# Kernel optimization log

Hardware: AMD Instinct MI355X
Metric: run time of the kernel (lower is better)

The kernel has to match this reference:

```python
import jax, jax.numpy as jnp
from jax import lax
import numpy as np

FW = 30          # edge_filter_width
THRESH = 0.015   # point_thresh
TOPK = 2000
SCALE = 4        # scale_cood2feat


def setup_inputs() -> dict:
    key = jax.random.key(0)
    k1, k2, k3 = jax.random.split(key, 3)
    B, H, W, C = 32, 384, 640, 128
    prob_nms = jax.random.uniform(k1, (B, 1, H, W), dtype=jnp.float32)
    featmap = jax.random.normal(k2, (B, C, H // SCALE, W // SCALE), dtype=jnp.float32)
    ratio = jax.random.uniform(k3, (B, 1), dtype=jnp.float32, minval=0.5, maxval=1.5)
    r_shape = jnp.tile(jnp.array([[H, W]], dtype=jnp.int64), (B, 1))
    return {"prob_nms": prob_nms, "featmap": featmap, "ratio": ratio, "r_shape": r_shape}


def _bilinear_gather(feat_hwc, pts_xy):
    # feat_hwc: [Hf, Wf, C]; pts_xy: [K, 2] float pixel coords (x, y)
    cf = pts_xy / SCALE
    x, y = cf[:, 0], cf[:, 1]
    x0 = jnp.floor(x).astype(jnp.int32)
    y0 = jnp.floor(y).astype(jnp.int32)
    x1, y1 = x0 + 1, y0 + 1
    fx1, fy1 = x1.astype(cf.dtype), y1.astype(cf.dtype)
    fx0, fy0 = x0.astype(cf.dtype), y0.astype(cf.dtype)
    wa = ((fx1 - x) * (fy1 - y))[:, None]
    wb = ((fx1 - x) * (y - fy0))[:, None]
    wc = ((x - fx0) * (fy1 - y))[:, None]
    wd = ((x - fx0) * (y - fy0))[:, None]
    Ia = feat_hwc[y0, x0]
    Ib = feat_hwc[y1, x0]
    Ic = feat_hwc[y0, x1]
    Id = feat_hwc[y1, x1]
    return Ia * wa + Ib * wb + Ic * wc + Id * wd


def _post_process_one(prob_hw, feat_hwc, ratio_s, rshape):
    H, W = prob_hw.shape
    iy = jnp.arange(H)[:, None]
    ix = jnp.arange(W)[None, :]
    # edge filtering: borders set to -1 == excluded from threshold test
    in_region = (iy >= FW) & (iy < rshape[0] - FW) & (ix >= FW) & (ix < rshape[1] - FW)
    mask = in_region & (prob_hw > THRESH)
    # compaction in row-major order (same order torch.where yields), padded with H*W
    lin = jnp.arange(H * W, dtype=jnp.int32)
    sentinel = jnp.int32(H * W)
    vals = jnp.where(mask.reshape(-1), lin, sentinel)
    neg_top, _ = lax.top_k(-vals, TOPK)   # smallest TOPK values, ascending
    idx = -neg_top
    valid = idx < sentinel
    idx_c = jnp.where(valid, idx, 0)
    yc = idx_c // W
    xc = idx_c % W
    pts_xy = jnp.stack([xc, yc], axis=1).astype(feat_hwc.dtype)  # flip -> (x, y)
    des = _bilinear_gather(feat_hwc, pts_xy)
    pts = pts_xy / ratio_s
    pts = jnp.where(valid[:, None], pts, jnp.zeros((), pts.dtype))
    des = jnp.where(valid[:, None], des, jnp.zeros((), des.dtype))
    return pts, des


def reference(prob_nms, featmap, ratio, r_shape):
    prob = prob_nms[:, 0]                       # [B, H, W]
    feat = jnp.transpose(featmap, (0, 2, 3, 1)) # [B, Hf, Wf, C]
    pts_t, des_t = jax.vmap(_post_process_one)(prob, feat, ratio[:, 0], r_shape)
    return pts_t, des_t
```

## Files before the change

### kernel.cpp

```cpp
#include <hip/hip_runtime.h>

#define NB 32
#define H 384
#define W 640
#define NC 128
#define FH 96
#define FWID 160
#define BORDER 30
#define PTHRESH 0.015f
#define TOPK 2000
#define HW (H * W)
#define NWAVE 4
#define NXIT 10

__device__ inline void load_rshape(const int* p32, int b, int* rs0, int* rs1) {
  const int a = p32[2 * b];
  const int c = p32[2 * b + 1];
  if (c == 0) {
    const long long* p64 = (const long long*)p32;
    *rs0 = (int)p64[2 * b];
    *rs1 = (int)p64[2 * b + 1];
  } else {
    *rs0 = a;
    *rs1 = c;
  }
}

__global__ __launch_bounds__(256) void compact_kernel(
    const float* __restrict__ prob, const int* __restrict__ rsp,
    int* __restrict__ out, int stride) {
  const int b = blockIdx.x;
  const int tid = threadIdx.x;
  const int lane = tid & 63;
  const int wv = tid >> 6;
  int rs0, rs1;
  load_rshape(rsp, b, &rs0, &rs1);
  const int ymax = rs0 - BORDER;
  const int xmax = rs1 - BORDER;
  const float* pb = prob + (size_t)b * HW;
  int* ob = out + (size_t)b * TOPK * stride;
  const unsigned long long ltmask = (1ull << lane) - 1ull;

  __shared__ int s_cnt[NWAVE];

  int chunk_base = 0;
  for (int row0 = BORDER; row0 < ymax && chunk_base < TOPK; row0 += NWAVE) {
    const int r = row0 + wv;
    unsigned long long mbs[NXIT];
    int cnt = 0;
    if (r < ymax) {
      const float* rowp = pb + r * W;
#pragma unroll
      for (int t = 0; t < NXIT; ++t) {
        const int x = t * 64 + lane;
        const bool m = (x >= BORDER) && (x < xmax) && (rowp[x] > PTHRESH);
        mbs[t] = __ballot(m);
        cnt += __popcll(mbs[t]);
      }
    } else {
#pragma unroll
      for (int t = 0; t < NXIT; ++t) mbs[t] = 0;
    }
    if (lane == 0) s_cnt[wv] = cnt;
    __syncthreads();
    int row_start = chunk_base;
    int total = 0;
#pragma unroll
    for (int j = 0; j < NWAVE; ++j) {
      const int cj = s_cnt[j];
      if (j < wv) row_start += cj;
      total += cj;
    }
    if (cnt > 0 && row_start < TOPK) {
      int rank = row_start;
      const int ibase = r * W;
#pragma unroll
      for (int t = 0; t < NXIT; ++t) {
        const unsigned long long mb = mbs[t];
        const bool m = (mb >> lane) & 1ull;
        const int pos = rank + __popcll(mb & ltmask);
        if (m && pos < TOPK) ob[(size_t)pos * stride] = ibase + t * 64 + lane;
        rank += __popcll(mb);
      }
    }
    chunk_base += total;
    __syncthreads();
  }
  const int filled = chunk_base < TOPK ? chunk_base : TOPK;
  for (int k = filled + tid; k < TOPK; k += 256)
    ob[(size_t)k * stride] = HW;
}

__global__ __launch_bounds__(128) void gather_kernel(
    const float* __restrict__ featmap, const float* __restrict__ ratio,
    const int* __restrict__ idx_base, int stride, float* __restrict__ pts,
    float* __restrict__ des) {
  const int k = blockIdx.x;
  const int b = blockIdx.y;
  const int pk = b * TOPK + k;
  const int c = threadIdx.x;

  const int idx = idx_base[(size_t)pk * stride];
  __syncthreads();

  const bool valid = (unsigned)idx < (unsigned)HW;
  const int ic = valid ? idx : 0;
  const int y = ic / W;
  const int x = ic - y * W;
  const int x0 = x >> 2;
  const int y0 = y >> 2;
  const float fx = (float)(x & 3) * 0.25f;
  const float fy = (float)(y & 3) * 0.25f;
  const float gx = 1.0f - fx, gy = 1.0f - fy;
  const float wa = gx * gy, wb = gx * fy, wc = fx * gy, wd = fx * fy;

  const float* fp = featmap + (((size_t)b * NC + c) * FH + y0) * FWID + x0;
  const float Ia = fp[0];
  const float Ic = fp[1];
  const float Ib = fp[FWID];
  const float Id = fp[FWID + 1];
  const float v = Ia * wa + Ib * wb + Ic * wc + Id * wd;
  des[(size_t)pk * NC + c] = valid ? v : 0.0f;

  if (c < 2) {
    const float p = (c == 0 ? (float)x : (float)y) / ratio[b];
    pts[pk * 2 + c] = valid ? p : 0.0f;
  }
}

extern "C" void kernel_launch(void* const* d_in, const int* in_sizes, int n_in,
                              void* d_out, int out_size, void* d_ws,
                              size_t ws_size, hipStream_t stream) {
  const float* prob = (const float*)d_in[0];
  const float* featmap = (const float*)d_in[1];
  const float* ratio = (const float*)d_in[2];
  const int* r_shape = (const int*)d_in[3];

  float* pts = (float*)d_out;
  float* des = pts + (size_t)NB * TOPK * 2;

  int* idx_base;
  int stride;
  if (ws_size >= (size_t)NB * TOPK * sizeof(int)) {
    idx_base = (int*)d_ws;
    stride = 1;
  } else {
    idx_base = (int*)des;
    stride = NC;
  }

  compact_kernel<<<NB, 256, 0, stream>>>(prob, r_shape, idx_base, stride);
  dim3 ggrid(TOPK, NB);
  gather_kernel<<<ggrid, 128, 0, stream>>>(featmap, ratio, idx_base, stride,
                                           pts, des);
}
```

Baseline: 370.2 us.

## Tile gather over 64 points per block with shared-memory transpose for coalescing

The gather kernel moves from one block per point, with one thread per channel, to one block per 64-point tile. Lanes now map to points and waves loop over channels, so neighbouring lanes read adjacent featmap addresses within a channel plane. Results are staged in a padded shared-memory tile and then written out channel-contiguous, so the descriptor stores stay coalesced. This cuts the block count and the scattered per-channel loads, at the cost of about 33 KB of shared memory per block and an extra barrier.

Measured after the change: 326.0 us. 1.14x faster.

```diff
diff --git a/kernel.cpp b/kernel.cpp
--- a/kernel.cpp
+++ b/kernel.cpp
@@ -12,6 +12,8 @@
 #define HW (H * W)
 #define NWAVE 4
 #define NXIT 10
+#define PTILE 64
+#define NTILE ((TOPK + PTILE - 1) / PTILE)
 
 __device__ inline void load_rshape(const int* p32, int b, int* rs0, int* rs1) {
   const int a = p32[2 * b];
@@ -91,18 +93,27 @@
     ob[(size_t)k * stride] = HW;
 }
 
-__global__ __launch_bounds__(128) void gather_kernel(
+__global__ __launch_bounds__(256) void gather_kernel(
     const float* __restrict__ featmap, const float* __restrict__ ratio,
     const int* __restrict__ idx_base, int stride, float* __restrict__ pts,
     float* __restrict__ des) {
-  const int k = blockIdx.x;
+  const int tile = blockIdx.x;
   const int b = blockIdx.y;
-  const int pk = b * TOPK + k;
-  const int c = threadIdx.x;
+  const int k0 = tile * PTILE;
+  const int npts = (TOPK - k0) < PTILE ? (TOPK - k0) : PTILE;
+  const int pk0 = b * TOPK + k0;
+  const int tid = threadIdx.x;
+  const int lane = tid & 63;
+  const int wv = tid >> 6;
 
-  const int idx = idx_base[(size_t)pk * stride];
+  __shared__ int s_idx[PTILE];
+  __shared__ float s_tile[NC][PTILE + 1];
+
+  if (tid < PTILE)
+    s_idx[tid] = (tid < npts) ? idx_base[(size_t)(pk0 + tid) * stride] : HW;
   __syncthreads();
 
+  const int idx = s_idx[lane];
   const bool valid = (unsigned)idx < (unsigned)HW;
   const int ic = valid ? idx : 0;
   const int y = ic / W;
@@ -112,20 +123,33 @@
   const float fx = (float)(x & 3) * 0.25f;
   const float fy = (float)(y & 3) * 0.25f;
   const float gx = 1.0f - fx, gy = 1.0f - fy;
-  const float wa = gx * gy, wb = gx * fy, wc = fx * gy, wd = fx * fy;
+  float wa = gx * gy, wb = gx * fy, wc = fx * gy, wd = fx * fy;
+  if (!valid) wa = wb = wc = wd = 0.0f;
 
-  const float* fp = featmap + (((size_t)b * NC + c) * FH + y0) * FWID + x0;
-  const float Ia = fp[0];
-  const float Ic = fp[1];
-  const float Ib = fp[FWID];
-  const float Id = fp[FWID + 1];
-  const float v = Ia * wa + Ib * wb + Ic * wc + Id * wd;
-  des[(size_t)pk * NC + c] = valid ? v : 0.0f;
+  const float* fp0 = featmap + (((size_t)b * NC) * FH + y0) * FWID + x0;
+#pragma unroll 4
+  for (int j = 0; j < NC / 4; ++j) {
+    const int c = wv * (NC / 4) + j;
+    const float* fp = fp0 + (size_t)c * (FH * FWID);
+    const float Ia = fp[0];
+    const float Ic = fp[1];
+    const float Ib = fp[FWID];
+    const float Id = fp[FWID + 1];
+    s_tile[c][lane] = Ia * wa + Ib * wb + Ic * wc + Id * wd;
+  }
 
-  if (c < 2) {
-    const float p = (c == 0 ? (float)x : (float)y) / ratio[b];
-    pts[pk * 2 + c] = valid ? p : 0.0f;
+  if (wv == 0 && lane < npts) {
+    const float r = ratio[b];
+    pts[(size_t)(pk0 + lane) * 2 + 0] = valid ? (float)x / r : 0.0f;
+    pts[(size_t)(pk0 + lane) * 2 + 1] = valid ? (float)y / r : 0.0f;
   }
+
+  __syncthreads();
+
+  float* db = des + (size_t)pk0 * NC;
+  const int c = tid & 127;
+  for (int k = tid >> 7; k < npts; k += 2)
+    db[(size_t)k * NC + c] = s_tile[c][k];
 }
 
 extern "C" void kernel_launch(void* const* d_in, const int* in_sizes, int n_in,
@@ -150,7 +174,7 @@
   }
 
   compact_kernel<<<NB, 256, 0, stream>>>(prob, r_shape, idx_base, stride);
-  dim3 ggrid(TOPK, NB);
-  gather_kernel<<<ggrid, 128, 0, stream>>>(featmap, ratio, idx_base, stride,
+  dim3 ggrid(NTILE, NB);
+  gather_kernel<<<ggrid, 256, 0, stream>>>(featmap, ratio, idx_base, stride,
                                            pts, des);
 }
```
